# Kernel optimization log

Hardware: AMD Instinct MI355X
Metric: run time of the kernel (lower is better)

## Reference

```python
import jax, jax.numpy as jnp
import numpy as np

B, S, E, H, HD, M = 4, 2048, 2048, 16, 128, 8192
EPS = 1e-5
SQRT_2_OVER_PI = 0.7978845608028654


def layer_norm(x, g, b):
    mu = jnp.mean(x, axis=-1, keepdims=True)
    var = jnp.mean(jnp.square(x - mu), axis=-1, keepdims=True)
    return (x - mu) * jax.lax.rsqrt(var + EPS) * g + b


def gelu_new(x):
    # tanh-approximate GELU (HF 'gelu_new')
    return 0.5 * x * (1.0 + jnp.tanh(SQRT_2_OVER_PI * (x + 0.044715 * x * x * x)))


def setup_inputs() -> dict:
    key = jax.random.key(0)
    ks = jax.random.split(key, 6)
    std = 0.02
    x = jax.random.normal(ks[0], (B, S, E), dtype=jnp.float32)
    mask = jnp.tril(jnp.ones((S, S), dtype=jnp.float32))  # causal, 1=allowed
    Wqkv = jax.random.normal(ks[1], (E, 3, H, HD), dtype=jnp.float32) * std
    bqkv = jnp.zeros((3, H, HD), dtype=jnp.float32)
    Wo = jax.random.normal(ks[2], (H, HD, E), dtype=jnp.float32) * std
    bo = jnp.zeros((E,), dtype=jnp.float32)
    Wfc = jax.random.normal(ks[3], (E, M), dtype=jnp.float32) * std
    bfc = jnp.zeros((M,), dtype=jnp.float32)
    Wp = jax.random.normal(ks[4], (M, E), dtype=jnp.float32) * std
    bp = jnp.zeros((E,), dtype=jnp.float32)
    return {
        'x': x, 'mask': mask,
        'ln1_g': jnp.ones((E,), jnp.float32), 'ln1_b': jnp.zeros((E,), jnp.float32),
        'Wqkv': Wqkv, 'bqkv': bqkv, 'Wo': Wo, 'bo': bo,
        'ln2_g': jnp.ones((E,), jnp.float32), 'ln2_b': jnp.zeros((E,), jnp.float32),
        'Wfc': Wfc, 'bfc': bfc, 'Wp': Wp, 'bp': bp,
        'layer_idx': 0,
    }


def reference(x, mask, ln1_g, ln1_b, Wqkv, bqkv, Wo, bo, ln2_g, ln2_b, Wfc, bfc, Wp, bp, layer_idx):
    # --- attention branch ---
    h = layer_norm(x, ln1_g, ln1_b)
    qkv = jnp.einsum('bse,ethd->btshd', h, Wqkv) + bqkv[:, None, :, :]  # [3,B?] -> actually [b,t,s,h,d]
    q, k, v = qkv[:, 0], qkv[:, 1], qkv[:, 2]  # each [b,s,h,d]
    scale = jax.lax.rsqrt(float(HD))  # scale_by_inverse_layer_idx=False
    q = q * scale
    scores = jnp.einsum('bqhd,bkhd->bhqk', q, k)
    scores = scores + (1.0 - mask) * -1e9  # mask broadcasts [q,k]
    w = jax.nn.softmax(scores, axis=-1).astype(x.dtype)  # dropout: inference, p=0
    attn = jnp.einsum('bhqk,bkhd->bqhd', w, v)
    attn = jnp.einsum('bqhd,hde->bqe', attn, Wo) + bo
    x = x + attn
    # --- MLP branch ---
    h2 = layer_norm(x, ln2_g, ln2_b)
    ff = gelu_new(jnp.einsum('bse,em->bsm', h2, Wfc) + bfc)
    ff = jnp.einsum('bsm,me->bse', ff, Wp) + bp
    return x + ff
```

## Files before the change

### kernel.cpp

```cpp
#include <hip/hip_runtime.h>
#include <hip/hip_bf16.h>
#include <math.h>


typedef __bf16 bf16;
typedef __attribute__((ext_vector_type(8))) __bf16 bf16x8;
typedef __attribute__((ext_vector_type(4))) float f32x4;

#define GLOBAL_AS __attribute__((address_space(1)))
#define LDS_AS __attribute__((address_space(3)))

__device__ __forceinline__ void gl_lds16(const bf16* g, bf16* l) {
  __builtin_amdgcn_global_load_lds((const GLOBAL_AS void*)g, (LDS_AS void*)l, 16, 0, 0);
}

struct Acc { f32x4 v[4][4]; };

__device__ __forceinline__ void gemm_core(const bf16* __restrict__ A, long lda,
                                          const bf16* __restrict__ Bt, long ldb,
                                          int m0, int n0, int kbeg, int kend,
                                          bf16* sa, bf16* sb, Acc& acc) {
  const int t    = threadIdx.x;
  const int lane = t & 63;
  const int w    = t >> 6;
  const int wm   = (w >> 1) << 6;
  const int wn   = (w & 1) << 6;
  const int quad = lane >> 4;
  const int l15  = lane & 15;
  const int rowA = t >> 2;
  const int kc   = (t & 3) << 3;

#pragma unroll
  for (int i = 0; i < 4; i++)
#pragma unroll
    for (int j = 0; j < 4; j++)
      acc.v[i][j] = f32x4{0.f, 0.f, 0.f, 0.f};

  bf16* sa_w0 = &sa[(w << 6) * 8];
  bf16* sa_w1 = &sa[(256 + (w << 6)) * 8];
  bf16* sb_w0 = &sb[(w << 6) * 8];
  bf16* sb_w1 = &sb[(256 + (w << 6)) * 8];

  for (int k0 = kbeg; k0 < kend; k0 += 32) {
    const bf16* ga = A + (long)(m0 + rowA) * lda + (k0 + kc);
    const bf16* gb = Bt + (long)(n0 + rowA) * ldb + (k0 + kc);
    gl_lds16(ga, sa_w0);
    gl_lds16(ga + 64 * lda, sa_w1);
    gl_lds16(gb, sb_w0);
    gl_lds16(gb + 64 * ldb, sb_w1);
    __syncthreads();

    bf16x8 af[4], bfv[4];
#pragma unroll
    for (int i = 0; i < 4; i++)
      af[i] = *(const bf16x8*)&sa[(wm + i * 16 + l15) * 32 + quad * 8];
#pragma unroll
    for (int j = 0; j < 4; j++)
      bfv[j] = *(const bf16x8*)&sb[(wn + j * 16 + l15) * 32 + quad * 8];
#pragma unroll
    for (int i = 0; i < 4; i++)
#pragma unroll
      for (int j = 0; j < 4; j++)
        acc.v[i][j] = __builtin_amdgcn_mfma_f32_16x16x32_bf16(af[i], bfv[j], acc.v[i][j], 0, 0, 0);
    __syncthreads();
  }
}

template <typename F>
__device__ __forceinline__ void epilogue(int m0, int n0, const Acc& acc, F f) {
  const int t = threadIdx.x;
  const int lane = t & 63;
  const int w = t >> 6;
  const int wm = (w >> 1) << 6, wn = (w & 1) << 6;
  const int quad = lane >> 4, l15 = lane & 15;
#pragma unroll
  for (int i = 0; i < 4; i++)
#pragma unroll
    for (int j = 0; j < 4; j++)
#pragma unroll
      for (int r = 0; r < 4; r++)
        f(m0 + wm + i * 16 + quad * 4 + r, n0 + wn + j * 16 + l15, acc.v[i][j][r]);
}

__global__ void k_transpose_cast(const float* __restrict__ src, bf16* __restrict__ dst,
                                 int R, int C) {
  __shared__ float tile[32][33];
  const int c0 = blockIdx.x << 5, r0 = blockIdx.y << 5;
  const int tx = threadIdx.x, ty = threadIdx.y;
  for (int i = ty; i < 32; i += 8)
    tile[i][tx] = src[(long)(r0 + i) * C + (c0 + tx)];
  __syncthreads();
  for (int i = ty; i < 32; i += 8)
    dst[(long)(c0 + i) * R + (r0 + tx)] = (bf16)tile[tx][i];
}

__global__ void k_layernorm(const float* __restrict__ x, const float* __restrict__ g,
                            const float* __restrict__ bta, bf16* __restrict__ out) {
  __shared__ float red[8];
  const long row = blockIdx.x;
  const float* xr = x + row * 2048;
  const int t = threadIdx.x;
  float4 a = reinterpret_cast<const float4*>(xr)[t];
  float4 b4 = reinterpret_cast<const float4*>(xr)[t + 256];
  float va[8] = {a.x, a.y, a.z, a.w, b4.x, b4.y, b4.z, b4.w};
  float s = 0.f, ss = 0.f;
#pragma unroll
  for (int i = 0; i < 8; i++) { s += va[i]; ss += va[i] * va[i]; }
#pragma unroll
  for (int o = 32; o > 0; o >>= 1) { s += __shfl_xor(s, o, 64); ss += __shfl_xor(ss, o, 64); }
  if ((t & 63) == 0) { red[t >> 6] = s; red[4 + (t >> 6)] = ss; }
  __syncthreads();
  s = red[0] + red[1] + red[2] + red[3];
  ss = red[4] + red[5] + red[6] + red[7];
  const float mu = s * (1.f / 2048.f);
  const float rstd = rsqrtf(ss * (1.f / 2048.f) - mu * mu + 1e-5f);
  bf16* op = out + row * 2048;
#pragma unroll
  for (int c = 0; c < 4; c++) {
    int i0 = t * 4 + c;
    op[i0] = (bf16)((va[c] - mu) * rstd * g[i0] + bta[i0]);
    int i1 = 1024 + t * 4 + c;
    op[i1] = (bf16)((va[4 + c] - mu) * rstd * g[i1] + bta[i1]);
  }
}

__global__ __launch_bounds__(256, 2) void k_gemm_qkv(
    const bf16* __restrict__ A, const bf16* __restrict__ Bt, const float* __restrict__ bias,
    bf16* __restrict__ q, bf16* __restrict__ k, bf16* __restrict__ v) {
  __shared__ bf16 sa[128 * 32], sb[128 * 32];
  const int m0 = blockIdx.y << 7, n0 = blockIdx.x << 7;
  Acc acc;
  gemm_core(A, 2048, Bt, 2048, m0, n0, 0, 2048, sa, sb, acc);
  epilogue(m0, n0, acc, [&](int row, int col, float val) {
    float vv = val + bias[col];
    const int which = col >> 11, hh = (col >> 7) & 15, d = col & 127;
    if (which == 0)
      q[((long)hh * 2048 + row) * 128 + d] = (bf16)(vv * 0.08838834764831845f);
    else if (which == 1)
      k[((long)hh * 2048 + row) * 128 + d] = (bf16)vv;
    else
      v[((long)hh * 128 + d) * 2048 + row] = (bf16)vv;
  });
}

__global__ __launch_bounds__(256, 2) void k_gemm_scores(
    const bf16* __restrict__ q, const bf16* __restrict__ kk, bf16* __restrict__ sc, int g) {
  const int m0 = blockIdx.y << 7, n0 = blockIdx.x << 7;
  if (n0 > m0) return;
  const int hp = blockIdx.z;
  __shared__ bf16 sa[128 * 32], sb[128 * 32];
  const bf16* qb = q + (long)(g * 8 + hp) * 2048 * 128;
  const bf16* kb = kk + (long)(g * 8 + hp) * 2048 * 128;
  Acc acc;
  gemm_core(qb, 128, kb, 128, m0, n0, 0, 128, sa, sb, acc);
  bf16* scp = sc + (long)hp * 2048 * 2048;
  epilogue(m0, n0, acc, [&](int row, int col, float val) {
    scp[(long)row * 2048 + col] = (bf16)val;
  });
}

__global__ void k_softmax(bf16* __restrict__ sc) {
  __shared__ float red[8];
  const int sq = blockIdx.x, hp = blockIdx.y;
  bf16* rowp = sc + ((long)hp * 2048 + sq) * 2048;
  const int L = sq + 1;
  const int Lpad = ((sq >> 7) + 1) << 7;
  const int t = threadIdx.x;
  float v[8];
  float mx = -3e38f;
#pragma unroll
  for (int i = 0; i < 8; i++) {
    int idx = t + (i << 8);
    v[i] = (idx < L) ? (float)rowp[idx] : -3e38f;
    mx = fmaxf(mx, v[i]);
  }
#pragma unroll
  for (int o = 32; o > 0; o >>= 1) mx = fmaxf(mx, __shfl_xor(mx, o, 64));
  if ((t & 63) == 0) red[t >> 6] = mx;
  __syncthreads();
  mx = fmaxf(fmaxf(red[0], red[1]), fmaxf(red[2], red[3]));
  float sum = 0.f;
#pragma unroll
  for (int i = 0; i < 8; i++) {
    int idx = t + (i << 8);
    if (idx < L) { v[i] = __expf(v[i] - mx); sum += v[i]; }
  }
#pragma unroll
  for (int o = 32; o > 0; o >>= 1) sum += __shfl_xor(sum, o, 64);
  if ((t & 63) == 0) red[4 + (t >> 6)] = sum;
  __syncthreads();
  sum = red[4] + red[5] + red[6] + red[7];
  const float inv = 1.f / sum;
#pragma unroll
  for (int i = 0; i < 8; i++) {
    int idx = t + (i << 8);
    if (idx < L) rowp[idx] = (bf16)(v[i] * inv);
    else if (idx < Lpad) rowp[idx] = (bf16)0.f;
  }
}

__global__ __launch_bounds__(256, 2) void k_gemm_pv(
    const bf16* __restrict__ sc, const bf16* __restrict__ v, bf16* __restrict__ attn, int g) {
  __shared__ bf16 sa[128 * 32], sb[128 * 32];
  const int m0 = blockIdx.x << 7;
  const int hp = blockIdx.y;
  const bf16* A = sc + (long)hp * 2048 * 2048;
  const bf16* Bt = v + (long)(g * 8 + hp) * 128 * 2048;
  Acc acc;
  gemm_core(A, 2048, Bt, 2048, m0, 0, 0, m0 + 128, sa, sb, acc);
  epilogue(m0, 0, acc, [&](int row, int col, float val) {
    attn[((long)row * 16 + (g * 8 + hp)) * 128 + col] = (bf16)val;
  });
}

__global__ __launch_bounds__(256, 2) void k_gemm_wo(
    const bf16* __restrict__ A, const bf16* __restrict__ Bt, const float* __restrict__ bias,
    const float* __restrict__ xin, float* __restrict__ x1) {
  __shared__ bf16 sa[128 * 32], sb[128 * 32];
  const int m0 = blockIdx.y << 7, n0 = blockIdx.x << 7;
  Acc acc;
  gemm_core(A, 2048, Bt, 2048, m0, n0, 0, 2048, sa, sb, acc);
  epilogue(m0, n0, acc, [&](int row, int col, float val) {
    long idx = (long)row * 2048 + col;
    x1[idx] = xin[idx] + val + bias[col];
  });
}

__global__ __launch_bounds__(256, 2) void k_gemm_fc(
    const bf16* __restrict__ A, const bf16* __restrict__ Bt, const float* __restrict__ bias,
    bf16* __restrict__ ff, int c) {
  __shared__ bf16 sa[128 * 32], sb[128 * 32];
  const int m0 = blockIdx.y << 7, n0 = blockIdx.x << 7;
  Acc acc;
  gemm_core(A, 2048, Bt, 2048, m0, n0, 0, 2048, sa, sb, acc);
  epilogue(m0, n0, acc, [&](int row, int col, float val) {
    float u = val + bias[c * 2048 + col];
    float cc = 0.7978845608028654f * (u + 0.044715f * u * u * u);
    float ge = 0.5f * u * (1.f + tanhf(cc));
    ff[(long)row * 2048 + col] = (bf16)ge;
  });
}

__global__ __launch_bounds__(256, 2) void k_gemm_wp(
    const bf16* __restrict__ A, const bf16* __restrict__ Bt, const float* __restrict__ bias,
    float* __restrict__ out, int addbias) {
  __shared__ bf16 sa[128 * 32], sb[128 * 32];
  const int m0 = blockIdx.y << 7, n0 = blockIdx.x << 7;
  Acc acc;
  gemm_core(A, 2048, Bt, 8192, m0, n0, 0, 2048, sa, sb, acc);
  epilogue(m0, n0, acc, [&](int row, int col, float val) {
    long idx = (long)row * 2048 + col;
    float b = addbias ? bias[col] : 0.f;
    out[idx] = out[idx] + val + b;
  });
}

extern "C" void kernel_launch(void* const* d_in, const int* in_sizes, int n_in,
                              void* d_out, int out_size, void* d_ws, size_t ws_size,
                              hipStream_t stream) {
  const float* x     = (const float*)d_in[0];
  const float* ln1_g = (const float*)d_in[2];
  const float* ln1_b = (const float*)d_in[3];
  const float* Wqkv  = (const float*)d_in[4];
  const float* bqkv  = (const float*)d_in[5];
  const float* Wo    = (const float*)d_in[6];
  const float* bo    = (const float*)d_in[7];
  const float* ln2_g = (const float*)d_in[8];
  const float* ln2_b = (const float*)d_in[9];
  const float* Wfc   = (const float*)d_in[10];
  const float* bfc   = (const float*)d_in[11];
  const float* Wp    = (const float*)d_in[12];
  const float* bp    = (const float*)d_in[13];
  float* out = (float*)d_out;

  char* p = (char*)d_ws;
  bf16* WqkvT = (bf16*)p; p += 6144L * 2048 * 2;
  bf16* WoT   = (bf16*)p; p += 2048L * 2048 * 2;
  bf16* WfcT  = (bf16*)p; p += 8192L * 2048 * 2;
  bf16* WpT   = (bf16*)p; p += 2048L * 8192 * 2;
  bf16* h     = (bf16*)p; p += 8192L * 2048 * 2;
  bf16* qb    = (bf16*)p; p += 16L * 2048 * 128 * 2;
  bf16* kb    = (bf16*)p; p += 16L * 2048 * 128 * 2;
  bf16* vb    = (bf16*)p; p += 16L * 2048 * 128 * 2;
  bf16* attnb = (bf16*)p; p += 16L * 2048 * 128 * 2;
  bf16* sc    = (bf16*)p; p += 8L * 2048 * 2048 * 2;
  bf16* h2 = h;
  bf16* ff = sc;

  dim3 tb(32, 8);
  k_transpose_cast<<<dim3(192, 64), tb, 0, stream>>>(Wqkv, WqkvT, 2048, 6144);
  k_transpose_cast<<<dim3(64, 64), tb, 0, stream>>>(Wo, WoT, 2048, 2048);
  k_transpose_cast<<<dim3(256, 64), tb, 0, stream>>>(Wfc, WfcT, 2048, 8192);
  k_transpose_cast<<<dim3(64, 256), tb, 0, stream>>>(Wp, WpT, 8192, 2048);

  k_layernorm<<<8192, 256, 0, stream>>>(x, ln1_g, ln1_b, h);

  for (int b = 0; b < 4; b++) {
    const bf16* hb = h + (long)b * 2048 * 2048;
    k_gemm_qkv<<<dim3(48, 16), 256, 0, stream>>>(hb, WqkvT, bqkv, qb, kb, vb);
    for (int g = 0; g < 2; g++) {
      k_gemm_scores<<<dim3(16, 16, 8), 256, 0, stream>>>(qb, kb, sc, g);
      k_softmax<<<dim3(2048, 8), 256, 0, stream>>>(sc);
      k_gemm_pv<<<dim3(16, 8), 256, 0, stream>>>(sc, vb, attnb, g);
    }
    k_gemm_wo<<<dim3(16, 16), 256, 0, stream>>>(attnb, WoT, bo,
                                                x + (long)b * 2048 * 2048,
                                                out + (long)b * 2048 * 2048);
  }

  k_layernorm<<<8192, 256, 0, stream>>>(out, ln2_g, ln2_b, h2);

  for (int c = 0; c < 4; c++) {
    k_gemm_fc<<<dim3(16, 64), 256, 0, stream>>>(h2, WfcT + (long)c * 2048 * 2048, bfc, ff, c);
    k_gemm_wp<<<dim3(16, 64), 256, 0, stream>>>(ff, WpT + (long)c * 2048, bp, out, c == 0);
  }
}
```

Baseline: 2.293 ms.

## Pack causal score buffer triangularly and restructure MLP chunking by rows

Attention scores are now stored in a packed lower-triangular layout per head. This lets all 16 heads fit in the workspace at once, so each batch needs one scores/softmax/PV launch instead of two groups, and the scores grid covers only the 136 causal tiles instead of launching and early-exiting the masked ones. The MLP now splits work by row halves (4096 rows, full 8192 hidden width) rather than four hidden-dimension chunks. Each Wp GEMM therefore runs the full K=8192 and does a single read-modify-write of the output instead of four accumulation passes. The trade-off is a larger intermediate ff buffer aliased onto the scores workspace and fewer but longer PV and Wp blocks, which may hurt load balance.

```diff
diff --git a/kernel.cpp b/kernel.cpp
--- a/kernel.cpp
+++ b/kernel.cpp
@@ -143,28 +143,37 @@
   });
 }
 
+#define SC_HEAD 2228224L
+
 __global__ __launch_bounds__(256, 2) void k_gemm_scores(
-    const bf16* __restrict__ q, const bf16* __restrict__ kk, bf16* __restrict__ sc, int g) {
-  const int m0 = blockIdx.y << 7, n0 = blockIdx.x << 7;
-  if (n0 > m0) return;
-  const int hp = blockIdx.z;
-  __shared__ bf16 sa[128 * 32], sb[128 * 32];
-  const bf16* qb = q + (long)(g * 8 + hp) * 2048 * 128;
-  const bf16* kb = kk + (long)(g * 8 + hp) * 2048 * 128;
-  Acc acc;
-  gemm_core(qb, 128, kb, 128, m0, n0, 0, 128, sa, sb, acc);
-  bf16* scp = sc + (long)hp * 2048 * 2048;
-  epilogue(m0, n0, acc, [&](int row, int col, float val) {
-    scp[(long)row * 2048 + col] = (bf16)val;
+    const bf16* __restrict__ q, const bf16* __restrict__ kk, bf16* __restrict__ sc) {
+  const int idx = blockIdx.x;
+  int m = (int)((sqrtf(8.f * idx + 1.f) - 1.f) * 0.5f);
+  if ((m + 1) * (m + 2) / 2 <= idx) m++;
+  if (m * (m + 1) / 2 > idx) m--;
+  const int n = idx - m * (m + 1) / 2;
+  const int h = blockIdx.z;
+  __shared__ bf16 sa[128 * 32], sb[128 * 32];
+  const bf16* qb = q + (long)h * 2048 * 128;
+  const bf16* kb = kk + (long)h * 2048 * 128;
+  Acc acc;
+  gemm_core(qb, 128, kb, 128, m << 7, n << 7, 0, 128, sa, sb, acc);
+  const long lda_m = (long)(m + 1) << 7;
+  bf16* scp = sc + (long)h * SC_HEAD + (long)m * (m + 1) * 8192;
+  const int mbase = m << 7;
+  epilogue(m << 7, n << 7, acc, [&](int row, int col, float val) {
+    scp[(long)(row - mbase) * lda_m + col] = (bf16)val;
   });
 }
 
 __global__ void k_softmax(bf16* __restrict__ sc) {
   __shared__ float red[8];
-  const int sq = blockIdx.x, hp = blockIdx.y;
-  bf16* rowp = sc + ((long)hp * 2048 + sq) * 2048;
+  const int sq = blockIdx.x, h = blockIdx.y;
+  const int mb = sq >> 7;
+  const int lda = (mb + 1) << 7;
+  bf16* rowp = sc + (long)h * SC_HEAD + (long)mb * (mb + 1) * 8192 + (long)(sq & 127) * lda;
   const int L = sq + 1;
-  const int Lpad = ((sq >> 7) + 1) << 7;
+  const int Lpad = lda;
   const int t = threadIdx.x;
   float v[8];
   float mx = -3e38f;
@@ -200,16 +209,18 @@
 }
 
 __global__ __launch_bounds__(256, 2) void k_gemm_pv(
-    const bf16* __restrict__ sc, const bf16* __restrict__ v, bf16* __restrict__ attn, int g) {
-  __shared__ bf16 sa[128 * 32], sb[128 * 32];
-  const int m0 = blockIdx.x << 7;
-  const int hp = blockIdx.y;
-  const bf16* A = sc + (long)hp * 2048 * 2048;
-  const bf16* Bt = v + (long)(g * 8 + hp) * 128 * 2048;
-  Acc acc;
-  gemm_core(A, 2048, Bt, 2048, m0, 0, 0, m0 + 128, sa, sb, acc);
-  epilogue(m0, 0, acc, [&](int row, int col, float val) {
-    attn[((long)row * 16 + (g * 8 + hp)) * 128 + col] = (bf16)val;
+    const bf16* __restrict__ sc, const bf16* __restrict__ v, bf16* __restrict__ attn) {
+  __shared__ bf16 sa[128 * 32], sb[128 * 32];
+  const int mb = blockIdx.x;
+  const int h = blockIdx.y;
+  const int lda = (mb + 1) << 7;
+  const bf16* A = sc + (long)h * SC_HEAD + (long)mb * (mb + 1) * 8192;
+  const bf16* Bt = v + (long)h * 128 * 2048;
+  Acc acc;
+  gemm_core(A, lda, Bt, 2048, 0, 0, 0, lda, sa, sb, acc);
+  const int rbase = mb << 7;
+  epilogue(0, 0, acc, [&](int row, int col, float val) {
+    attn[((long)(rbase + row) * 16 + h) * 128 + col] = (bf16)val;
   });
 }
 
@@ -228,30 +239,29 @@
 
 __global__ __launch_bounds__(256, 2) void k_gemm_fc(
     const bf16* __restrict__ A, const bf16* __restrict__ Bt, const float* __restrict__ bias,
-    bf16* __restrict__ ff, int c) {
+    bf16* __restrict__ ff) {
   __shared__ bf16 sa[128 * 32], sb[128 * 32];
   const int m0 = blockIdx.y << 7, n0 = blockIdx.x << 7;
   Acc acc;
   gemm_core(A, 2048, Bt, 2048, m0, n0, 0, 2048, sa, sb, acc);
   epilogue(m0, n0, acc, [&](int row, int col, float val) {
-    float u = val + bias[c * 2048 + col];
+    float u = val + bias[col];
     float cc = 0.7978845608028654f * (u + 0.044715f * u * u * u);
     float ge = 0.5f * u * (1.f + tanhf(cc));
-    ff[(long)row * 2048 + col] = (bf16)ge;
+    ff[(long)row * 8192 + col] = (bf16)ge;
   });
 }
 
 __global__ __launch_bounds__(256, 2) void k_gemm_wp(
     const bf16* __restrict__ A, const bf16* __restrict__ Bt, const float* __restrict__ bias,
-    float* __restrict__ out, int addbias) {
+    float* __restrict__ out) {
   __shared__ bf16 sa[128 * 32], sb[128 * 32];
   const int m0 = blockIdx.y << 7, n0 = blockIdx.x << 7;
   Acc acc;
-  gemm_core(A, 2048, Bt, 8192, m0, n0, 0, 2048, sa, sb, acc);
+  gemm_core(A, 8192, Bt, 8192, m0, n0, 0, 8192, sa, sb, acc);
   epilogue(m0, n0, acc, [&](int row, int col, float val) {
     long idx = (long)row * 2048 + col;
-    float b = addbias ? bias[col] : 0.f;
-    out[idx] = out[idx] + val + b;
+    out[idx] = out[idx] + val + bias[col];
   });
 }
 
@@ -283,7 +293,7 @@
   bf16* kb    = (bf16*)p; p += 16L * 2048 * 128 * 2;
   bf16* vb    = (bf16*)p; p += 16L * 2048 * 128 * 2;
   bf16* attnb = (bf16*)p; p += 16L * 2048 * 128 * 2;
-  bf16* sc    = (bf16*)p; p += 8L * 2048 * 2048 * 2;
+  bf16* sc    = (bf16*)p; p += 16L * SC_HEAD * 2;
   bf16* h2 = h;
   bf16* ff = sc;
 
@@ -298,11 +308,9 @@
   for (int b = 0; b < 4; b++) {
     const bf16* hb = h + (long)b * 2048 * 2048;
     k_gemm_qkv<<<dim3(48, 16), 256, 0, stream>>>(hb, WqkvT, bqkv, qb, kb, vb);
-    for (int g = 0; g < 2; g++) {
-      k_gemm_scores<<<dim3(16, 16, 8), 256, 0, stream>>>(qb, kb, sc, g);
-      k_softmax<<<dim3(2048, 8), 256, 0, stream>>>(sc);
-      k_gemm_pv<<<dim3(16, 8), 256, 0, stream>>>(sc, vb, attnb, g);
-    }
+    k_gemm_scores<<<dim3(136, 1, 16), 256, 0, stream>>>(qb, kb, sc);
+    k_softmax<<<dim3(2048, 16), 256, 0, stream>>>(sc);
+    k_gemm_pv<<<dim3(16, 16), 256, 0, stream>>>(sc, vb, attnb);
     k_gemm_wo<<<dim3(16, 16), 256, 0, stream>>>(attnb, WoT, bo,
                                                 x + (long)b * 2048 * 2048,
                                                 out + (long)b * 2048 * 2048);
@@ -310,8 +318,9 @@
 
   k_layernorm<<<8192, 256, 0, stream>>>(out, ln2_g, ln2_b, h2);
 
-  for (int c = 0; c < 4; c++) {
-    k_gemm_fc<<<dim3(16, 64), 256, 0, stream>>>(h2, WfcT + (long)c * 2048 * 2048, bfc, ff, c);
-    k_gemm_wp<<<dim3(16, 64), 256, 0, stream>>>(ff, WpT + (long)c * 2048, bp, out, c == 0);
-  }
-}
+  for (int r = 0; r < 2; r++) {
+    const bf16* h2r = h2 + (long)r * 4096 * 2048;
+    k_gemm_fc<<<dim3(64, 32), 256, 0, stream>>>(h2r, WfcT, bfc, ff);
+    k_gemm_wp<<<dim3(16, 32), 256, 0, stream>>>(ff, WpT, bp, out + (long)r * 4096 * 2048);
+  }
+}
```

New measurement: 2.018 ms. -12.0%, faster.
